# Optimization experiments

Measured on AMD Instinct MI355X. Metric: run time of the kernel, lower is better.

Reference implementation:

```python
import jax, jax.numpy as jnp
import numpy as np

B, S, ENC, HID = 2, 2048, 2048, 2048
HQ, HKV, D = 8, 4, 256
SOFTCAP = 50.0
SCALING = float(256) ** -0.5  # query_pre_attn_scalar ** -0.5
EPS = 1e-6
NEG = -1e9  # finite stand-in for -inf in additive masks


def _rms_norm(x, w, eps=EPS):
    # GemmaRMSNorm: fp32 compute, scale by (1 + weight)
    xf = x.astype(jnp.float32)
    n = xf * jax.lax.rsqrt(jnp.mean(xf * xf, axis=-1, keepdims=True) + eps)
    return (n * (1.0 + w.astype(jnp.float32))).astype(x.dtype)


def _rotate_half(x):
    x1, x2 = jnp.split(x, 2, axis=-1)
    return jnp.concatenate([-x2, x1], axis=-1)


def _apply_rope(q, k, cos, sin):
    # q,k: [B, H, S, D]; cos,sin: [1, S, D] -> unsqueeze head dim
    c, s = cos[:, None, :, :], sin[:, None, :, :]
    return q * c + _rotate_half(q) * s, k * c + _rotate_half(k) * s


def setup_inputs() -> dict:
    key = jax.random.key(0)
    ks = jax.random.split(key, 8)
    hidden_states = jax.random.normal(ks[0], (B, S, HID), jnp.float32)
    encoder_hidden_states = jax.random.normal(ks[1], (B, ENC, HID), jnp.float32)
    # RoPE tables (base 10000)
    pos = jnp.arange(S, dtype=jnp.float32)
    inv_freq = 1.0 / (10000.0 ** (jnp.arange(0, D, 2, dtype=jnp.float32) / D))
    freqs = pos[:, None] * inv_freq[None, :]                 # [S, D/2]
    emb = jnp.concatenate([freqs, freqs], axis=-1)           # [S, D]
    cos = jnp.cos(emb)[None]                                 # [1, S, D]
    sin = jnp.sin(emb)[None]
    # merged additive mask: causal over self part, fully visible cross part
    causal = jnp.where(jnp.arange(S)[:, None] >= jnp.arange(S)[None, :], 0.0, NEG)
    mask = jnp.concatenate([causal, jnp.zeros((S, ENC), jnp.float32)], axis=-1)
    merged_attention_mask = mask[None, None].astype(jnp.float32)  # [1,1,S,S+ENC]
    w = 0.02
    Wq = jax.random.normal(ks[2], (HQ * D, HID), jnp.float32) * w
    Wk = jax.random.normal(ks[3], (HKV * D, HID), jnp.float32) * w
    Wv = jax.random.normal(ks[4], (HKV * D, HID), jnp.float32) * w
    Wo = jax.random.normal(ks[5], (HID, HQ * D), jnp.float32) * w
    q_norm_w = jnp.zeros((D,), jnp.float32)
    k_norm_w = jnp.zeros((D,), jnp.float32)
    return dict(hidden_states=hidden_states, encoder_hidden_states=encoder_hidden_states,
                cos=cos, sin=sin, merged_attention_mask=merged_attention_mask,
                Wq=Wq, Wk=Wk, Wv=Wv, Wo=Wo, q_norm_w=q_norm_w, k_norm_w=k_norm_w)


def reference(hidden_states, encoder_hidden_states, cos, sin, merged_attention_mask,
              Wq, Wk, Wv, Wo, q_norm_w, k_norm_w):
    b, s, _ = hidden_states.shape
    enc = encoder_hidden_states.shape[1]
    n_rep = HQ // HKV
    # projections
    q = hidden_states @ Wq.T                                 # [B,S,HQ*D]
    k_self = hidden_states @ Wk.T
    v_self = hidden_states @ Wv.T
    k_cross = encoder_hidden_states @ Wk.T
    v_cross = encoder_hidden_states @ Wv.T
    q = q.reshape(b, s, HQ, D).transpose(0, 2, 1, 3)         # [B,HQ,S,D]
    k_self = k_self.reshape(b, s, HKV, D).transpose(0, 2, 1, 3)
    v_self = v_self.reshape(b, s, HKV, D).transpose(0, 2, 1, 3)
    k_cross = k_cross.reshape(b, enc, HKV, D).transpose(0, 2, 1, 3)
    v_cross = v_cross.reshape(b, enc, HKV, D).transpose(0, 2, 1, 3)
    # QK RMSNorm + RoPE (RoPE only on self q/k)
    q = _rms_norm(q, q_norm_w)
    k_self = _rms_norm(k_self, k_norm_w)
    k_cross = _rms_norm(k_cross, k_norm_w)
    q, k_self = _apply_rope(q, k_self, cos, sin)
    # merged KV + GQA repeat
    k = jnp.concatenate([k_self, k_cross], axis=2)           # [B,HKV,S+ENC,D]
    v = jnp.concatenate([v_self, v_cross], axis=2)
    k = jnp.repeat(k, n_rep, axis=1)                         # [B,HQ,S+ENC,D]
    v = jnp.repeat(v, n_rep, axis=1)
    # eager softcapped attention
    scores = jnp.einsum('bhqd,bhkd->bhqk', q, k) * SCALING
    scores = SOFTCAP * jnp.tanh(scores / SOFTCAP)
    scores = scores + merged_attention_mask
    probs = jax.nn.softmax(scores, axis=-1)
    attn = jnp.einsum('bhqk,bhkd->bhqd', probs, v)           # [B,HQ,S,D]
    attn = attn.transpose(0, 2, 1, 3).reshape(b, s, HQ * D)
    return attn @ Wo.T
```

## Files before the change

kernel.cpp:

```cpp
#include <hip/hip_runtime.h>
#include <cstdint>

typedef __attribute__((ext_vector_type(8))) short bf16x8;
typedef __attribute__((ext_vector_type(4))) float f32x4;

#define B_ 2
#define S_ 2048
#define ENC_ 2048
#define HID_ 2048
#define HQ_ 8
#define HKV_ 4
#define D_ 256
#define L_ 4096

__device__ __forceinline__ short f2bf(float f) {
  uint32_t u = __builtin_bit_cast(uint32_t, f);
  u = (u + 0x7fffu + ((u >> 16) & 1u)) >> 16;
  return (short)u;
}
__device__ __forceinline__ float bf2f(short s) {
  uint32_t u = ((uint32_t)(uint16_t)s) << 16;
  return __builtin_bit_cast(float, u);
}

__device__ __forceinline__ void llds16(const void* g, void* s) {
  __builtin_amdgcn_global_load_lds(
      (const __attribute__((address_space(1))) void*)(__builtin_bit_cast(uintptr_t, g)),
      (__attribute__((address_space(3))) void*)(uint32_t)(__builtin_bit_cast(uintptr_t, s)),
      16, 0, 0);
}

__global__ __launch_bounds__(256) void cvt_f32_bf16(const float* __restrict__ in,
                                                    short* __restrict__ out, int n) {
  int i = (blockIdx.x * 256 + threadIdx.x) * 4;
  if (i >= n) return;
  float4 v = *(const float4*)(in + i);
  short4 r;
  r.x = f2bf(v.x); r.y = f2bf(v.y); r.z = f2bf(v.z); r.w = f2bf(v.w);
  *(short4*)(out + i) = r;
}

template <int BF16OUT>
__global__ __launch_bounds__(256, 2)
void gemm_bt(const short* __restrict__ A, const short* __restrict__ Bw,
             void* __restrict__ Cout, int M, int N, int K) {
  __shared__ __align__(16) short As[128 * 32];
  __shared__ __align__(16) short Bs[128 * 32];
  const int t = threadIdx.x;
  const int w = t >> 6;
  const int l = t & 63;
  const int lr = l & 15;
  const int lq = l >> 4;
  const int bm = blockIdx.y * 128;
  const int bn = blockIdx.x * 128;
  const int wm = (w & 1) * 64;
  const int wn = (w >> 1) * 64;

  f32x4 acc[4][4];
#pragma unroll
  for (int i = 0; i < 4; i++)
#pragma unroll
    for (int j = 0; j < 4; j++) acc[i][j] = f32x4{0.f, 0.f, 0.f, 0.f};

  const int srow = 32 * w + (l >> 2);
  const int scol = (l & 3) * 8;
  const short* gA = A + (size_t)(bm + srow) * K + scol;
  const short* gB = Bw + (size_t)(bn + srow) * K + scol;
  short* sA = &As[srow * 32 + scol];
  short* sB = &Bs[srow * 32 + scol];

  for (int k0 = 0; k0 < K; k0 += 32) {
    llds16(gA + k0, sA);
    llds16(gA + k0 + (size_t)16 * K, sA + 16 * 32);
    llds16(gB + k0, sB);
    llds16(gB + k0 + (size_t)16 * K, sB + 16 * 32);
    __syncthreads();
    bf16x8 af[4], bfr[4];
#pragma unroll
    for (int mi = 0; mi < 4; mi++)
      af[mi] = *(const bf16x8*)&As[(wm + 16 * mi + lr) * 32 + lq * 8];
#pragma unroll
    for (int ni = 0; ni < 4; ni++)
      bfr[ni] = *(const bf16x8*)&Bs[(wn + 16 * ni + lr) * 32 + lq * 8];
    __syncthreads();
#pragma unroll
    for (int mi = 0; mi < 4; mi++)
#pragma unroll
      for (int ni = 0; ni < 4; ni++)
        acc[mi][ni] =
            __builtin_amdgcn_mfma_f32_16x16x32_bf16(af[mi], bfr[ni], acc[mi][ni], 0, 0, 0);
  }

#pragma unroll
  for (int mi = 0; mi < 4; mi++)
#pragma unroll
    for (int ni = 0; ni < 4; ni++)
#pragma unroll
      for (int r = 0; r < 4; r++) {
        int row = bm + wm + 16 * mi + lq * 4 + r;
        int col = bn + wn + 16 * ni + lr;
        float v = acc[mi][ni][r];
        if (BF16OUT)
          ((short*)Cout)[(size_t)row * N + col] = f2bf(v);
        else
          ((float*)Cout)[(size_t)row * N + col] = v;
      }
}

__global__ __launch_bounds__(256)
void norm_rope(const short* __restrict__ src, int src_ld, int col0, int H,
               short* __restrict__ dst, int dstL, int pos_off, int do_rope, int kswz,
               const float* __restrict__ wn, const float* __restrict__ cosp,
               const float* __restrict__ sinp) {
  __shared__ float sh[256];
  __shared__ float red[4];
  int bid = blockIdx.x;
  int s = bid & (S_ - 1);
  int h = (bid >> 11) % H;
  int b = (bid >> 11) / H;
  int d = threadIdx.x;
  int w = d >> 6, l = d & 63;
  float x = bf2f(src[(size_t)(b * S_ + s) * src_ld + col0 + h * D_ + d]);
  float ss = x * x;
#pragma unroll
  for (int off = 32; off; off >>= 1) ss += __shfl_xor(ss, off, 64);
  if (l == 0) red[w] = ss;
  __syncthreads();
  float tot = red[0] + red[1] + red[2] + red[3];
  float y = x * rsqrtf(tot * (1.0f / D_) + 1e-6f) * (1.0f + wn[d]);
  float outv = y;
  if (do_rope) {
    sh[d] = y;
    __syncthreads();
    float c = cosp[s * D_ + d];
    float sn = sinp[s * D_ + d];
    outv = (d < 128) ? (y * c - sh[d + 128] * sn) : (y * c + sh[d - 128] * sn);
  }
  int dd = d;
  if (kswz) dd = (((d >> 3) ^ (s & 7)) << 3) | (d & 7);
  dst[((size_t)(b * H + h) * dstL + pos_off + s) * D_ + dd] = f2bf(outv);
}

__global__ __launch_bounds__(256)
void v_transpose(const short* __restrict__ qkv_self, const short* __restrict__ kv_cross,
                 short* __restrict__ Vt) {
  __shared__ __align__(16) short tile[64][72];
  int bid = blockIdx.x;
  int dt = bid & 3;
  int lt = (bid >> 2) & 63;
  int h = (bid >> 8) & 3;
  int b = bid >> 10;
  int t = threadIdx.x;
  int rl = t >> 2;
  int cc = (t & 3) * 16;
  int l = lt * 64 + rl;
  const short* src;
  if (lt < 32)
    src = qkv_self + (size_t)(b * S_ + l) * 4096 + 3072 + h * D_ + dt * 64 + cc;
  else
    src = kv_cross + (size_t)(b * ENC_ + (l - S_)) * 2048 + 1024 + h * D_ + dt * 64 + cc;
  *(bf16x8*)&tile[rl][cc] = *(const bf16x8*)src;
  *(bf16x8*)&tile[rl][cc + 8] = *(const bf16x8*)(src + 8);
  __syncthreads();
  int dl = t >> 2;
  int lc = (t & 3) * 16;
  bf16x8 v0, v1;
#pragma unroll
  for (int j = 0; j < 8; j++) {
    v0[j] = tile[lc + j][dl];
    v1[j] = tile[lc + 8 + j][dl];
  }
  int d = dt * 64 + dl;
  int e = dl & 7;
  int c0 = 2 * (t & 3);
  short* rowp = Vt + ((size_t)(b * HKV_ + h) * D_ + d) * (size_t)L_ + lt * 64;
  *(bf16x8*)(rowp + ((c0 ^ e) * 8)) = v0;
  *(bf16x8*)(rowp + (((c0 + 1) ^ e) * 8)) = v1;
}

__global__ __launch_bounds__(256)
void flash_attn(const short* __restrict__ Q, const short* __restrict__ K,
                const short* __restrict__ Vt, short* __restrict__ part0,
                short* __restrict__ part1, float* __restrict__ lsum) {
  __shared__ __align__(16) short Ks[64 * 256];
  __shared__ __align__(16) short Vs[256 * 64];
  __shared__ __align__(16) short Ps[4][16 * 72];
  int t = threadIdx.x, w = t >> 6, l = t & 63;
  int lr = l & 15, lq = l >> 4, x7 = lr & 7;
  int bid = blockIdx.x;
  int pair = bid >> 5;
  int p = (bid >> 4) & 1;
  int bh = bid & 15;
  int b = bh >> 3, h = bh & 7, hk = h >> 1;
  short* op = p ? part1 : part0;

  const short* Kbase = K + (size_t)(b * HKV_ + hk) * L_ * D_;
  const short* Vbase = Vt + (size_t)(b * HKV_ + hk) * (size_t)D_ * L_;

  int gi = p;
  const int lenA = pair + 33;

  for (int phase = 0; phase < 2; ++phase) {
    int qt = phase ? (31 - pair) : pair;
    int q0 = qt * 64;
    int nself = qt + 1;
    int base = phase ? lenA : 0;
    int lim = base + nself + 32;
    int qglob = q0 + 16 * w + lr;

    bf16x8 qf[8];
    {
      const short* qb = Q + ((size_t)(b * HQ_ + h) * S_ + qglob) * D_ + lq * 8;
#pragma unroll
      for (int kf = 0; kf < 8; kf++) qf[kf] = *(const bf16x8*)(qb + kf * 32);
    }
    f32x4 o[16];
#pragma unroll
    for (int i = 0; i < 16; i++) o[i] = f32x4{0.f, 0.f, 0.f, 0.f};
    float lacc = 0.f;

    for (; gi < lim; gi += 2) {
      int local = gi - base;
      int j = (local < nself) ? local : (local - nself + 32);
      int k0 = j * 64;
      bool diag = (j == qt);

      {
        const short* kg = Kbase + (size_t)(k0 + 16 * w) * 256 + l * 8;
        short* ks = &Ks[16 * w * 256];
#pragma unroll
        for (int i = 0; i < 8; i++) llds16(kg + i * 512, ks + i * 512);
        const short* vg = Vbase + (size_t)(64 * w + (l >> 3)) * L_ + k0 + (l & 7) * 8;
        short* vs = &Vs[64 * w * 64];
#pragma unroll
        for (int i = 0; i < 8; i++) llds16(vg + (size_t)(8 * i) * L_, vs + i * 512);
      }
      __syncthreads();

      f32x4 sc[4];
#pragma unroll
      for (int nt = 0; nt < 4; nt++) sc[nt] = f32x4{0.f, 0.f, 0.f, 0.f};
#pragma unroll
      for (int kf = 0; kf < 8; kf++) {
#pragma unroll
        for (int nt = 0; nt < 4; nt++) {
          bf16x8 a = *(const bf16x8*)&Ks[(nt * 16 + lr) * 256 + (((4 * kf + lq) ^ x7) * 8)];
          sc[nt] = __builtin_amdgcn_mfma_f32_16x16x32_bf16(a, qf[kf], sc[nt], 0, 0, 0);
        }
      }

#pragma unroll
      for (int nt = 0; nt < 4; nt++) {
        float pe[4];
#pragma unroll
        for (int r = 0; r < 4; r++) {
          float s = sc[nt][r];
          float u = s * (1.0f / 800.0f);
          float t2 = u * u;
          float poly = 1.0f + t2 * (-0.33333334f + t2 * (0.13333334f + t2 * (-0.05396825f)));
          float cap = s * 0.0625f * poly;
          float pv = __expf(cap);
          if (diag && (k0 + nt * 16 + 4 * lq + r > qglob)) pv = 0.f;
          pe[r] = pv;
          lacc += pv;
        }
        uint32_t lo = (uint32_t)(uint16_t)f2bf(pe[0]) | ((uint32_t)(uint16_t)f2bf(pe[1]) << 16);
        uint32_t hi = (uint32_t)(uint16_t)f2bf(pe[2]) | ((uint32_t)(uint16_t)f2bf(pe[3]) << 16);
        *(uint2*)&Ps[w][lr * 72 + nt * 16 + lq * 4] = uint2{lo, hi};
      }

#pragma unroll
      for (int kf2 = 0; kf2 < 2; kf2++) {
        bf16x8 pb = *(const bf16x8*)&Ps[w][lr * 72 + kf2 * 32 + lq * 8];
#pragma unroll
        for (int dt = 0; dt < 16; dt++) {
          bf16x8 va = *(const bf16x8*)&Vs[(dt * 16 + lr) * 64 + (((4 * kf2 + lq) ^ x7) * 8)];
          o[dt] = __builtin_amdgcn_mfma_f32_16x16x32_bf16(va, pb, o[dt], 0, 0, 0);
        }
      }
      __syncthreads();
    }

    size_t orow = ((size_t)b * S_ + qglob) * (HQ_ * D_) + h * D_;
#pragma unroll
    for (int dt = 0; dt < 16; dt++) {
      short4 st;
      st.x = f2bf(o[dt][0]);
      st.y = f2bf(o[dt][1]);
      st.z = f2bf(o[dt][2]);
      st.w = f2bf(o[dt][3]);
      *(short4*)(op + orow + dt * 16 + 4 * lq) = st;
    }
    float lrow = lacc;
    lrow += __shfl_xor(lrow, 16, 64);
    lrow += __shfl_xor(lrow, 32, 64);
    if (lq == 0)
      lsum[(((size_t)p * B_ + b) * HQ_ + h) * S_ + qglob] = lrow;
  }
}

__global__ __launch_bounds__(256)
void combine2(const short* __restrict__ p0, const short* __restrict__ p1,
              const float* __restrict__ lsum, short* __restrict__ out) {
  int tid = blockIdx.x * 256 + threadIdx.x;
  int flat = tid * 4;
  int h = (flat >> 8) & 7;
  int s = (flat >> 11) & 2047;
  int b = flat >> 22;
  size_t sbase = ((size_t)b * HQ_ + h) * S_ + s;
  const size_t SP = (size_t)B_ * HQ_ * S_;
  float inv = 1.0f / (lsum[sbase] + lsum[SP + sbase]);
  short4 a = *(const short4*)(p0 + (size_t)flat);
  short4 c = *(const short4*)(p1 + (size_t)flat);
  short4 r;
  r.x = f2bf((bf2f(a.x) + bf2f(c.x)) * inv);
  r.y = f2bf((bf2f(a.y) + bf2f(c.y)) * inv);
  r.z = f2bf((bf2f(a.z) + bf2f(c.z)) * inv);
  r.w = f2bf((bf2f(a.w) + bf2f(c.w)) * inv);
  *(short4*)(out + flat) = r;
}

extern "C" void kernel_launch(void* const* d_in, const int* in_sizes, int n_in, void* d_out,
                              int out_size, void* d_ws, size_t ws_size, hipStream_t stream) {
  (void)in_sizes; (void)n_in; (void)out_size; (void)ws_size;
  const float* hidden = (const float*)d_in[0];
  const float* encoder = (const float*)d_in[1];
  const float* cosp = (const float*)d_in[2];
  const float* sinp = (const float*)d_in[3];
  const float* Wq = (const float*)d_in[5];
  const float* Wk = (const float*)d_in[6];
  const float* Wv = (const float*)d_in[7];
  const float* Wo = (const float*)d_in[8];
  const float* qnw = (const float*)d_in[9];
  const float* knw = (const float*)d_in[10];

  short* ws = (short*)d_ws;
  short* hs_bf = ws;
  short* enc_bf = ws + 8388608;
  short* wqkv_bf = ws + 16777216;
  short* wo_bf = ws + 25165824;
  short* qkv_self = ws + 29360128;
  short* kv_cross = ws + 46137344;
  short* Kb = ws + 54525952;
  short* Vtb = ws + 62914560;
  short* attn_b = hs_bf;
  short* Qb = enc_bf;
  short* part0 = qkv_self;
  short* part1 = qkv_self + 8388608;
  float* lsum = (float*)d_out;

  cvt_f32_bf16<<<8192, 256, 0, stream>>>(hidden, hs_bf, 8388608);
  cvt_f32_bf16<<<8192, 256, 0, stream>>>(encoder, enc_bf, 8388608);
  cvt_f32_bf16<<<4096, 256, 0, stream>>>(Wq, wqkv_bf, 4194304);
  cvt_f32_bf16<<<2048, 256, 0, stream>>>(Wk, wqkv_bf + 4194304, 2097152);
  cvt_f32_bf16<<<2048, 256, 0, stream>>>(Wv, wqkv_bf + 6291456, 2097152);
  cvt_f32_bf16<<<4096, 256, 0, stream>>>(Wo, wo_bf, 4194304);

  gemm_bt<1><<<dim3(32, 32), 256, 0, stream>>>(hs_bf, wqkv_bf, qkv_self, 4096, 4096, 2048);
  gemm_bt<1><<<dim3(16, 32), 256, 0, stream>>>(enc_bf, wqkv_bf + (size_t)2048 * 2048, kv_cross,
                                               4096, 2048, 2048);

  norm_rope<<<32768, 256, 0, stream>>>(qkv_self, 4096, 0, 8, Qb, 2048, 0, 1, 0, qnw, cosp, sinp);
  norm_rope<<<16384, 256, 0, stream>>>(qkv_self, 4096, 2048, 4, Kb, 4096, 0, 1, 1, knw, cosp, sinp);
  norm_rope<<<16384, 256, 0, stream>>>(kv_cross, 2048, 0, 4, Kb, 4096, 2048, 0, 1, knw, cosp, sinp);

  v_transpose<<<2048, 256, 0, stream>>>(qkv_self, kv_cross, Vtb);

  flash_attn<<<512, 256, 0, stream>>>(Qb, Kb, Vtb, part0, part1, lsum);
  combine2<<<8192, 256, 0, stream>>>(part0, part1, lsum, attn_b);

  gemm_bt<0><<<dim3(16, 32), 256, 0, stream>>>(attn_b, wo_bf, d_out, 4096, 2048, 2048);
}
```

Before: 591.2 us.

## Double-buffer flash attention K/V tiles with 32-key stages and async prefetch

```diff
diff --git a/kernel.cpp b/kernel.cpp
--- a/kernel.cpp
+++ b/kernel.cpp
@@ -28,6 +28,12 @@
       (const __attribute__((address_space(1))) void*)(__builtin_bit_cast(uintptr_t, g)),
       (__attribute__((address_space(3))) void*)(uint32_t)(__builtin_bit_cast(uintptr_t, s)),
       16, 0, 0);
+}
+
+__device__ __forceinline__ void wg_barrier() {
+  asm volatile("" ::: "memory");
+  __builtin_amdgcn_s_barrier();
+  asm volatile("" ::: "memory");
 }
 
 __global__ __launch_bounds__(256) void cvt_f32_bf16(const float* __restrict__ in,
@@ -171,22 +177,25 @@
     v1[j] = tile[lc + 8 + j][dl];
   }
   int d = dt * 64 + dl;
-  int e = dl & 7;
+  int e3 = dl & 3;
   int c0 = 2 * (t & 3);
+  int c1 = c0 + 1;
+  int p0 = (c0 & 4) | ((c0 ^ e3) & 3);
+  int p1 = (c1 & 4) | ((c1 ^ e3) & 3);
   short* rowp = Vt + ((size_t)(b * HKV_ + h) * D_ + d) * (size_t)L_ + lt * 64;
-  *(bf16x8*)(rowp + ((c0 ^ e) * 8)) = v0;
-  *(bf16x8*)(rowp + (((c0 + 1) ^ e) * 8)) = v1;
+  *(bf16x8*)(rowp + p0 * 8) = v0;
+  *(bf16x8*)(rowp + p1 * 8) = v1;
 }
 
 __global__ __launch_bounds__(256)
 void flash_attn(const short* __restrict__ Q, const short* __restrict__ K,
                 const short* __restrict__ Vt, short* __restrict__ part0,
                 short* __restrict__ part1, float* __restrict__ lsum) {
-  __shared__ __align__(16) short Ks[64 * 256];
-  __shared__ __align__(16) short Vs[256 * 64];
-  __shared__ __align__(16) short Ps[4][16 * 72];
+  __shared__ __align__(16) short Ks[2][32 * 256];
+  __shared__ __align__(16) short Vs[2][256 * 32];
+  __shared__ __align__(16) short Ps[4][16 * 40];
   int t = threadIdx.x, w = t >> 6, l = t & 63;
-  int lr = l & 15, lq = l >> 4, x7 = lr & 7;
+  int lr = l & 15, lq = l >> 4, x7 = lr & 7, x3 = lr & 3;
   int bid = blockIdx.x;
   int pair = bid >> 5;
   int p = (bid >> 4) & 1;
@@ -196,6 +205,17 @@
 
   const short* Kbase = K + (size_t)(b * HKV_ + hk) * L_ * D_;
   const short* Vbase = Vt + (size_t)(b * HKV_ + hk) * (size_t)D_ * L_;
+
+  auto stage = [&](int bufi, int k0) {
+    const short* kg = Kbase + (size_t)(k0 + 8 * w + (l >> 5)) * 256 + (l & 31) * 8;
+    short* ks = &Ks[bufi][8 * w * 256 + l * 8];
+#pragma unroll
+    for (int i = 0; i < 4; i++) llds16(kg + i * 512, ks + i * 512);
+    const short* vg = Vbase + (size_t)(64 * w + (l >> 2)) * (size_t)L_ + k0 + (l & 3) * 8;
+    short* vs = &Vs[bufi][64 * w * 32 + l * 8];
+#pragma unroll
+    for (int i = 0; i < 4; i++) llds16(vg + (size_t)(16 * i) * L_, vs + i * 512);
+  };
 
   int gi = p;
   const int lenA = pair + 33;
@@ -219,67 +239,83 @@
     for (int i = 0; i < 16; i++) o[i] = f32x4{0.f, 0.f, 0.f, 0.f};
     float lacc = 0.f;
 
-    for (; gi < lim; gi += 2) {
-      int local = gi - base;
+    int gcur = gi, u = 0, buf = 0;
+    {
+      int local = gcur - base;
       int j = (local < nself) ? local : (local - nself + 32);
-      int k0 = j * 64;
+      stage(0, j * 64);
+    }
+
+    while (true) {
+      int gn = gcur, un = u + 1;
+      if (un == 2) { un = 0; gn = gcur + 2; }
+      bool hn = (gn < lim);
+      if (hn) {
+        int localn = gn - base;
+        int jn = (localn < nself) ? localn : (localn - nself + 32);
+        stage(buf ^ 1, jn * 64 + 32 * un);
+        asm volatile("s_waitcnt vmcnt(8)" ::: "memory");
+      } else {
+        asm volatile("s_waitcnt vmcnt(0)" ::: "memory");
+      }
+      wg_barrier();
+
+      int local = gcur - base;
+      int j = (local < nself) ? local : (local - nself + 32);
+      int k0 = j * 64 + 32 * u;
       bool diag = (j == qt);
-
-      {
-        const short* kg = Kbase + (size_t)(k0 + 16 * w) * 256 + l * 8;
-        short* ks = &Ks[16 * w * 256];
-#pragma unroll
-        for (int i = 0; i < 8; i++) llds16(kg + i * 512, ks + i * 512);
-        const short* vg = Vbase + (size_t)(64 * w + (l >> 3)) * L_ + k0 + (l & 7) * 8;
-        short* vs = &Vs[64 * w * 64];
-#pragma unroll
-        for (int i = 0; i < 8; i++) llds16(vg + (size_t)(8 * i) * L_, vs + i * 512);
-      }
-      __syncthreads();
-
-      f32x4 sc[4];
-#pragma unroll
-      for (int nt = 0; nt < 4; nt++) sc[nt] = f32x4{0.f, 0.f, 0.f, 0.f};
+      const short* KsB = &Ks[buf][0];
+      const short* VsB = &Vs[buf][0];
+
+      f32x4 sc[2];
+      sc[0] = f32x4{0.f, 0.f, 0.f, 0.f};
+      sc[1] = f32x4{0.f, 0.f, 0.f, 0.f};
+      __builtin_amdgcn_s_setprio(1);
 #pragma unroll
       for (int kf = 0; kf < 8; kf++) {
 #pragma unroll
-        for (int nt = 0; nt < 4; nt++) {
-          bf16x8 a = *(const bf16x8*)&Ks[(nt * 16 + lr) * 256 + (((4 * kf + lq) ^ x7) * 8)];
+        for (int nt = 0; nt < 2; nt++) {
+          bf16x8 a = *(const bf16x8*)&KsB[(nt * 16 + lr) * 256 + (((4 * kf + lq) ^ x7) * 8)];
           sc[nt] = __builtin_amdgcn_mfma_f32_16x16x32_bf16(a, qf[kf], sc[nt], 0, 0, 0);
         }
       }
-
-#pragma unroll
-      for (int nt = 0; nt < 4; nt++) {
+      __builtin_amdgcn_s_setprio(0);
+
+#pragma unroll
+      for (int nt = 0; nt < 2; nt++) {
         float pe[4];
 #pragma unroll
         for (int r = 0; r < 4; r++) {
           float s = sc[nt][r];
-          float u = s * (1.0f / 800.0f);
-          float t2 = u * u;
-          float poly = 1.0f + t2 * (-0.33333334f + t2 * (0.13333334f + t2 * (-0.05396825f)));
-          float cap = s * 0.0625f * poly;
+          float t2 = s * s * 1.5625e-6f;
+          float hh = fmaf(t2, -0.0033730157f, 0.0083333338f);
+          hh = fmaf(t2, hh, -0.020833334f);
+          hh = fmaf(t2, hh, 0.0625f);
+          float cap = s * hh;
           float pv = __expf(cap);
           if (diag && (k0 + nt * 16 + 4 * lq + r > qglob)) pv = 0.f;
           pe[r] = pv;
-          lacc += pv;
         }
+        lacc += (pe[0] + pe[1]) + (pe[2] + pe[3]);
         uint32_t lo = (uint32_t)(uint16_t)f2bf(pe[0]) | ((uint32_t)(uint16_t)f2bf(pe[1]) << 16);
         uint32_t hi = (uint32_t)(uint16_t)f2bf(pe[2]) | ((uint32_t)(uint16_t)f2bf(pe[3]) << 16);
-        *(uint2*)&Ps[w][lr * 72 + nt * 16 + lq * 4] = uint2{lo, hi};
+        *(uint2*)&Ps[w][lr * 40 + nt * 16 + lq * 4] = uint2{lo, hi};
       }
 
-#pragma unroll
-      for (int kf2 = 0; kf2 < 2; kf2++) {
-        bf16x8 pb = *(const bf16x8*)&Ps[w][lr * 72 + kf2 * 32 + lq * 8];
-#pragma unroll
-        for (int dt = 0; dt < 16; dt++) {
-          bf16x8 va = *(const bf16x8*)&Vs[(dt * 16 + lr) * 64 + (((4 * kf2 + lq) ^ x7) * 8)];
-          o[dt] = __builtin_amdgcn_mfma_f32_16x16x32_bf16(va, pb, o[dt], 0, 0, 0);
-        }
+      bf16x8 pb = *(const bf16x8*)&Ps[w][lr * 40 + lq * 8];
+      __builtin_amdgcn_s_setprio(1);
+#pragma unroll
+      for (int dt = 0; dt < 16; dt++) {
+        bf16x8 va = *(const bf16x8*)&VsB[(dt * 16 + lr) * 32 + ((lq ^ x3) * 8)];
+        o[dt] = __builtin_amdgcn_mfma_f32_16x16x32_bf16(va, pb, o[dt], 0, 0, 0);
       }
-      __syncthreads();
+      __builtin_amdgcn_s_setprio(0);
+
+      wg_barrier();
+      if (!hn) break;
+      gcur = gn; u = un; buf ^= 1;
     }
+    gi = gcur + 2;
 
     size_t orow = ((size_t)b * S_ + qglob) * (HQ_ * D_) + h * D_;
 #pragma unroll
```

Result: no change. 585.7 us (-0.9%).
